# Kernel tuning notes

Measured on AMD Instinct MI355X. Metric: run time of the kernel, lower is better.

Reference implementation:

```python
import jax, jax.numpy as jnp
import numpy as np

N = 131072
H = 64
CMB_RADIUS_KM = 3485.0


def setup_inputs() -> dict:
    key = jax.random.key(0)
    ks = jax.random.split(key, 8)
    phi = jax.random.uniform(ks[0], (N, 1), jnp.float32, 0.0, 2.0 * np.pi)
    # keep theta away from the poles so sin(theta) != 0
    theta = jax.random.uniform(ks[1], (N, 1), jnp.float32, 0.1, np.pi - 0.1)
    radius = jnp.full((N, 1), CMB_RADIUS_KM, dtype=jnp.float32)
    horiz_theta = jax.random.normal(ks[2], (N, 1), jnp.float32) * 0.01
    horiz_phi = jax.random.normal(ks[3], (N, 1), jnp.float32) * 0.01
    br = jax.random.normal(ks[4], (N, 1), jnp.float32) * 100.0
    W1 = jax.random.normal(ks[5], (2, H), jnp.float32) / np.sqrt(2.0)
    b1 = jnp.zeros((H,), jnp.float32)
    W2 = jax.random.normal(ks[6], (H, H), jnp.float32) / np.sqrt(H)
    b2 = jnp.zeros((H,), jnp.float32)
    W3 = jax.random.normal(ks[7], (H, 1), jnp.float32) / np.sqrt(H)
    b3 = jnp.zeros((1,), jnp.float32)
    return dict(phi=phi, theta=theta, radius=radius, horiz_theta=horiz_theta,
                horiz_phi=horiz_phi, br=br, W1=W1, b1=b1, W2=W2, b2=b2, W3=W3, b3=b3)


def reference(phi, theta, radius, horiz_theta, horiz_phi, br, W1, b1, W2, b2, W3, b3):
    sin = jnp.sin

    # per-point scalar network; input order matches torch.cat([phi, theta], dim=1)
    def T(p, t):
        x = jnp.stack([p, t])
        h = jnp.tanh(x @ W1 + b1)
        h = jnp.tanh(h @ W2 + b2)
        return (h @ W3 + b3)[0]

    dTp = jax.grad(T, 0)
    dTt = jax.grad(T, 1)

    # In the torch code T = model(X) and P = model(X) are the same function,
    # so T_x == P_x and the flows simplify to:
    def u_th(p, t):
        return dTp(p, t) / sin(t) + dTt(p, t)

    def u_ph(p, t):
        return dTp(p, t) / sin(t) - dTt(p, t)

    # nested derivatives exactly as the chained autograd.grad calls
    u_th_t = jax.grad(lambda p, t: -u_th(p, t) * sin(t), 1)            # u_theta_theta
    u_th_tt = jax.grad(lambda p, t: u_th_t(p, t) * sin(t), 1)          # u_theta_theta_theta
    u_th_p = jax.grad(lambda p, t: -u_th(p, t), 0)                     # u_theta_phi
    u_th_pp = jax.grad(u_th_p, 0)                                      # u_theta_phi_phi
    u_ph_t = jax.grad(lambda p, t: u_ph(p, t) * sin(t), 1)             # u_phi_theta
    u_ph_tt = jax.grad(lambda p, t: u_ph_t(p, t) * sin(t), 1)          # u_phi_theta_theta
    u_ph_p = jax.grad(u_ph, 0)                                         # u_phi_phi
    u_ph_pp = jax.grad(u_ph_p, 0)                                      # u_phi_phi_phi

    def per_point(p, t):
        return (u_th(p, t), u_ph(p, t), u_th_t(p, t), u_th_tt(p, t),
                u_th_pp(p, t), u_ph_tt(p, t), u_ph_p(p, t), u_ph_pp(p, t))

    vals = jax.vmap(per_point)(phi.ravel(), theta.ravel())
    ut, up, utt, uttt, utpp, uphtt, upp, uppp = [v.reshape(-1, 1) for v in vals]

    s = sin(theta)
    div_uh = (utt + upp) / (radius * s)
    u_theta_lap = s / radius ** 2 * uttt + utpp / (radius * s) ** 2
    u_phi_lap = s / radius ** 2 * uphtt + uppp / (radius * s) ** 2
    comp = s * (u_theta_lap ** 2 + u_phi_lap ** 2)
    sv_out = -(ut * horiz_theta + up * horiz_phi) - br * div_uh
    tg_con = div_uh - ut * jnp.tan(theta) / radius
    return (ut, up, div_uh, sv_out, tg_con, comp)
```

## Files before the change

kernel.cpp:

```cpp
#include <hip/hip_runtime.h>

#define NH 64

typedef _Float16 half8 __attribute__((ext_vector_type(8)));
typedef float float4v __attribute__((ext_vector_type(4)));

__device__ __forceinline__ float fast_tanh(float x) {
  float ax = fabsf(x);
  float e  = __expf(-2.0f * ax);
  float y  = (1.0f - e) * __builtin_amdgcn_rcpf(1.0f + e);
  return copysignf(y, x);
}

__global__ void prep_B(const float* __restrict__ W2, _Float16* __restrict__ ws) {
  int i = blockIdx.x * 256 + threadIdx.x;
  if (i >= 2 * 4096) return;
  int s = i >> 12;
  int off = i & 4095;
  int nt = off >> 10;
  int ks = (off >> 9) & 1;
  int ln = (off >> 3) & 63;
  int jj = off & 7;
  int h = ks * 32 + (ln >> 4) * 8 + jj;
  int j = nt * 16 + (ln & 15);
  float w2 = W2[h * NH + j];
  _Float16 hi = (_Float16)w2;
  ws[(s * 8 + nt * 2 + ks) * 512 + ln * 8 + jj] =
      (s == 0) ? hi : (_Float16)(w2 - (float)hi);
}

__device__ __forceinline__ half8 ldB(const _Float16* ws, int s, int nt, int ks, int lane) {
  return *(const half8*)(ws + (s * 8 + nt * 2 + ks) * 512 + lane * 8);
}

__global__ __launch_bounds__(256) __attribute__((amdgpu_waves_per_eu(2, 2)))
void pinn_mfma(
    const float* __restrict__ phi, const float* __restrict__ theta,
    const float* __restrict__ radius, const float* __restrict__ hth,
    const float* __restrict__ hph, const float* __restrict__ br,
    const float* __restrict__ W1, const float* __restrict__ b1,
    const float* __restrict__ b2, const float* __restrict__ W3,
    const _Float16* __restrict__ Bws, float* __restrict__ out, int n) {
  const int lane = threadIdx.x & 63;
  const int wave = threadIdx.x >> 6;
  const int tile = blockIdx.x * 4 + wave;
  const int quad = lane >> 4, col = lane & 15;
  const int pbase = tile * 16;
  if (pbase >= n) return;

  float p = phi[pbase + col], t = theta[pbase + col];
  half8 A0h[2], A0l[2], A1h[2], A1l[2], A2h[2], A2l[2];
  half8 A3[2], A4[2], A5[2], A6[2], A7[2], A8[2], A9[2];
#pragma unroll
  for (int ks = 0; ks < 2; ++ks) {
#pragma unroll
    for (int jj = 0; jj < 8; ++jj) {
      int h = ks * 32 + quad * 8 + jj;
      float a = W1[h], b = W1[NH + h];
      float z = fmaf(p, a, fmaf(t, b, b1[h]));
      float y = fast_tanh(z);
      float f1 = fmaf(-y, y, 1.0f);
      float f2a = y * f1;
      float f3 = f1 * fmaf(-6.0f, f1, 4.0f);
      float a2 = a * a, ab = a * b, b2v_ = b * b;
      float v1 = f1 * a, v2 = f1 * b;
      _Float16 yh = (_Float16)y;
      _Float16 v1h = (_Float16)v1;
      _Float16 v2h = (_Float16)v2;
      A0h[ks][jj] = yh;   A0l[ks][jj] = (_Float16)(y - (float)yh);
      A1h[ks][jj] = v1h;  A1l[ks][jj] = (_Float16)(v1 - (float)v1h);
      A2h[ks][jj] = v2h;  A2l[ks][jj] = (_Float16)(v2 - (float)v2h);
      A3[ks][jj] = (_Float16)(f2a * (-2.0f * a2));
      A4[ks][jj] = (_Float16)(f2a * (-2.0f * ab));
      A5[ks][jj] = (_Float16)(f2a * (-2.0f * b2v_));
      A6[ks][jj] = (_Float16)(f3 * (a2 * a));
      A7[ks][jj] = (_Float16)(f3 * (a2 * b));
      A8[ks][jj] = (_Float16)(f3 * (a * b2v_));
      A9[ks][jj] = (_Float16)(f3 * (b2v_ * b));
    }
  }

  float4v Tacc[9];
#pragma unroll
  for (int x = 0; x < 9; ++x) Tacc[x] = (float4v){0.f, 0.f, 0.f, 0.f};

#pragma unroll
  for (int nt = 0; nt < 4; ++nt) {
    float4v acc[10];
#pragma unroll
    for (int k = 0; k < 10; ++k) acc[k] = (float4v){0.f, 0.f, 0.f, 0.f};
#pragma unroll
    for (int ks = 0; ks < 2; ++ks) {
      half8 bh = ldB(Bws, 0, nt, ks, lane);
      half8 bl = ldB(Bws, 1, nt, ks, lane);
      acc[0] = __builtin_amdgcn_mfma_f32_16x16x32_f16(A0h[ks], bh, acc[0], 0, 0, 0);
      acc[0] = __builtin_amdgcn_mfma_f32_16x16x32_f16(A0l[ks], bh, acc[0], 0, 0, 0);
      acc[0] = __builtin_amdgcn_mfma_f32_16x16x32_f16(A0h[ks], bl, acc[0], 0, 0, 0);
      acc[1] = __builtin_amdgcn_mfma_f32_16x16x32_f16(A1h[ks], bh, acc[1], 0, 0, 0);
      acc[1] = __builtin_amdgcn_mfma_f32_16x16x32_f16(A1l[ks], bh, acc[1], 0, 0, 0);
      acc[1] = __builtin_amdgcn_mfma_f32_16x16x32_f16(A1h[ks], bl, acc[1], 0, 0, 0);
      acc[2] = __builtin_amdgcn_mfma_f32_16x16x32_f16(A2h[ks], bh, acc[2], 0, 0, 0);
      acc[2] = __builtin_amdgcn_mfma_f32_16x16x32_f16(A2l[ks], bh, acc[2], 0, 0, 0);
      acc[2] = __builtin_amdgcn_mfma_f32_16x16x32_f16(A2h[ks], bl, acc[2], 0, 0, 0);
      acc[3] = __builtin_amdgcn_mfma_f32_16x16x32_f16(A3[ks], bh, acc[3], 0, 0, 0);
      acc[4] = __builtin_amdgcn_mfma_f32_16x16x32_f16(A4[ks], bh, acc[4], 0, 0, 0);
      acc[5] = __builtin_amdgcn_mfma_f32_16x16x32_f16(A5[ks], bh, acc[5], 0, 0, 0);
      acc[6] = __builtin_amdgcn_mfma_f32_16x16x32_f16(A6[ks], bh, acc[6], 0, 0, 0);
      acc[7] = __builtin_amdgcn_mfma_f32_16x16x32_f16(A7[ks], bh, acc[7], 0, 0, 0);
      acc[8] = __builtin_amdgcn_mfma_f32_16x16x32_f16(A8[ks], bh, acc[8], 0, 0, 0);
      acc[9] = __builtin_amdgcn_mfma_f32_16x16x32_f16(A9[ks], bh, acc[9], 0, 0, 0);
    }
    float b2v = b2[nt * 16 + col];
    float w3v = W3[nt * 16 + col];
#pragma unroll
    for (int r = 0; r < 4; ++r) {
      float z0 = acc[0][r] + b2v;
      float y2 = fast_tanh(z0);
      float g1 = fmaf(-y2, y2, 1.0f);
      float g2 = -2.0f * (y2 * g1);
      float g3 = g1 * fmaf(-6.0f, g1, 4.0f);
      float gp = acc[1][r], gt = acc[2][r];
      float gpp = acc[3][r], gpt = acc[4][r], gtt = acc[5][r];
      float zppp = acc[6][r], zppt = acc[7][r], zptt = acc[8][r], zttt = acc[9][r];
      float gp2 = gp * gp, gt2 = gt * gt;
      Tacc[0][r] = fmaf(w3v, g1 * gp, Tacc[0][r]);
      Tacc[1][r] = fmaf(w3v, g1 * gt, Tacc[1][r]);
      Tacc[2][r] = fmaf(w3v, fmaf(g2, gp2, g1 * gpp), Tacc[2][r]);
      Tacc[3][r] = fmaf(w3v, fmaf(g2, gp * gt, g1 * gpt), Tacc[3][r]);
      Tacc[4][r] = fmaf(w3v, fmaf(g2, gt2, g1 * gtt), Tacc[4][r]);
      Tacc[5][r] = fmaf(w3v, fmaf(g3, gp2 * gp, fmaf(3.0f * g2, gp * gpp, g1 * zppp)), Tacc[5][r]);
      Tacc[6][r] = fmaf(w3v, fmaf(g3, gp2 * gt, fmaf(g2, fmaf(2.0f, gp * gpt, gt * gpp), g1 * zppt)), Tacc[6][r]);
      Tacc[7][r] = fmaf(w3v, fmaf(g3, gp * gt2, fmaf(g2, fmaf(2.0f, gt * gpt, gp * gtt), g1 * zptt)), Tacc[7][r]);
      Tacc[8][r] = fmaf(w3v, fmaf(g3, gt2 * gt, fmaf(3.0f * g2, gt * gtt, g1 * zttt)), Tacc[8][r]);
    }
  }

#pragma unroll
  for (int x = 0; x < 9; ++x) {
#pragma unroll
    for (int r = 0; r < 4; ++r) {
      float v = Tacc[x][r];
      v += __shfl_xor(v, 1, 16);
      v += __shfl_xor(v, 2, 16);
      v += __shfl_xor(v, 4, 16);
      v += __shfl_xor(v, 8, 16);
      Tacc[x][r] = v;
    }
  }

  int rsel = col & 3;
  float T[9];
#pragma unroll
  for (int x = 0; x < 9; ++x) {
    float4v v = Tacc[x];
    T[x] = (rsel == 0) ? v[0] : (rsel == 1) ? v[1] : (rsel == 2) ? v[2] : v[3];
  }
  float Tp = T[0], Tt = T[1], Tpp = T[2], Tpt = T[3], Ttt = T[4];
  float Tppp = T[5], Tppt = T[6], Tptt = T[7], Tttt = T[8];

  int pi = pbase + quad * 4 + rsel;
  float t2 = theta[pi];
  float s = sinf(t2), c = cosf(t2);
  float inv_s = 1.0f / s;
  float inv_s2 = inv_s * inv_s;

  float A = Tp * inv_s + Tt;
  float D = Tp * inv_s - Tt;
  float q1 = Tpt * inv_s - Tp * c * inv_s2;
  float A_t = q1 + Ttt;
  float D_t = q1 - Ttt;
  float q2 = Tptt * inv_s - 2.0f * Tpt * c * inv_s2
           + Tp * (s * s + 2.0f * c * c) * inv_s2 * inv_s;
  float A_tt = q2 + Tttt;
  float D_tt = q2 - Tttt;
  float A_pp = Tppp * inv_s + Tppt;
  float D_p  = Tpp * inv_s - Tpt;
  float D_pp = Tppp * inv_s - Tppt;

  float utt   = -(A_t * s + A * c);
  float uttt  = -(A_tt * s + 2.0f * A_t * c - A * s) * s + utt * c;
  float utpp  = -A_pp;
  float upht  = D_t * s + D * c;
  float uphtt = (D_tt * s + 2.0f * D_t * c - D * s) * s + upht * c;
  float upp   = D_p;
  float uppp  = D_pp;

  float r = radius[pi];
  float inv_r = 1.0f / r;
  float inv_r2 = inv_r * inv_r;
  float div_uh = (utt + upp) * inv_r * inv_s;
  float lap_t = s * inv_r2 * uttt + utpp * inv_s2 * inv_r2;
  float lap_p = s * inv_r2 * uphtt + uppp * inv_s2 * inv_r2;
  float comp = s * (lap_t * lap_t + lap_p * lap_p);
  float sv = -(A * hth[pi] + D * hph[pi]) - br[pi] * div_uh;
  float tg = div_uh - A * (s / c) * inv_r;

  if (col < 4) {
    out[pi]         = A;
    out[n + pi]     = D;
    out[2 * n + pi] = div_uh;
    out[3 * n + pi] = sv;
    out[4 * n + pi] = tg;
    out[5 * n + pi] = comp;
  }
}

extern "C" void kernel_launch(void* const* d_in, const int* in_sizes, int n_in,
                              void* d_out, int out_size, void* d_ws, size_t ws_size,
                              hipStream_t stream) {
  const float* phi    = (const float*)d_in[0];
  const float* theta  = (const float*)d_in[1];
  const float* radius = (const float*)d_in[2];
  const float* hth    = (const float*)d_in[3];
  const float* hph    = (const float*)d_in[4];
  const float* br     = (const float*)d_in[5];
  const float* W1     = (const float*)d_in[6];
  const float* b1     = (const float*)d_in[7];
  const float* W2     = (const float*)d_in[8];
  const float* b2     = (const float*)d_in[9];
  const float* W3     = (const float*)d_in[10];
  (void)ws_size; (void)n_in; (void)out_size;

  _Float16* Bws = (_Float16*)d_ws;
  float* out = (float*)d_out;
  int n = in_sizes[0];

  prep_B<<<(2 * 4096 + 255) / 256, 256, 0, stream>>>(W2, Bws);
  int ntiles = (n + 15) / 16;
  int nblocks = (ntiles + 3) / 4;
  pinn_mfma<<<nblocks, 256, 0, stream>>>(
      phi, theta, radius, hth, hph, br, W1, b1, b2, W3, Bws, out, n);
}
```

Baseline: 113.2 us.

## Use transpose-reduce across lanes and fast sincos/rcp in epilogue

```diff
diff --git a/kernel.cpp b/kernel.cpp
--- a/kernel.cpp
+++ b/kernel.cpp
@@ -60,9 +60,10 @@
       float z = fmaf(p, a, fmaf(t, b, b1[h]));
       float y = fast_tanh(z);
       float f1 = fmaf(-y, y, 1.0f);
-      float f2a = y * f1;
       float f3 = f1 * fmaf(-6.0f, f1, 4.0f);
-      float a2 = a * a, ab = a * b, b2v_ = b * b;
+      float na = -2.0f * (y * f1);
+      float a2 = a * a, ab = a * b, bb = b * b;
+      float f3a2 = f3 * a2, f3bb = f3 * bb;
       float v1 = f1 * a, v2 = f1 * b;
       _Float16 yh = (_Float16)y;
       _Float16 v1h = (_Float16)v1;
@@ -70,13 +71,13 @@
       A0h[ks][jj] = yh;   A0l[ks][jj] = (_Float16)(y - (float)yh);
       A1h[ks][jj] = v1h;  A1l[ks][jj] = (_Float16)(v1 - (float)v1h);
       A2h[ks][jj] = v2h;  A2l[ks][jj] = (_Float16)(v2 - (float)v2h);
-      A3[ks][jj] = (_Float16)(f2a * (-2.0f * a2));
-      A4[ks][jj] = (_Float16)(f2a * (-2.0f * ab));
-      A5[ks][jj] = (_Float16)(f2a * (-2.0f * b2v_));
-      A6[ks][jj] = (_Float16)(f3 * (a2 * a));
-      A7[ks][jj] = (_Float16)(f3 * (a2 * b));
-      A8[ks][jj] = (_Float16)(f3 * (a * b2v_));
-      A9[ks][jj] = (_Float16)(f3 * (b2v_ * b));
+      A3[ks][jj] = (_Float16)(na * a2);
+      A4[ks][jj] = (_Float16)(na * ab);
+      A5[ks][jj] = (_Float16)(na * bb);
+      A6[ks][jj] = (_Float16)(f3a2 * a);
+      A7[ks][jj] = (_Float16)(f3a2 * b);
+      A8[ks][jj] = (_Float16)(f3bb * a);
+      A9[ks][jj] = (_Float16)(f3bb * b);
     }
   }
 
@@ -135,33 +136,34 @@
     }
   }
 
-#pragma unroll
-  for (int x = 0; x < 9; ++x) {
-#pragma unroll
-    for (int r = 0; r < 4; ++r) {
-      float v = Tacc[x][r];
-      v += __shfl_xor(v, 1, 16);
-      v += __shfl_xor(v, 2, 16);
-      v += __shfl_xor(v, 4, 16);
-      v += __shfl_xor(v, 8, 16);
-      Tacc[x][r] = v;
-    }
-  }
-
-  int rsel = col & 3;
   float T[9];
 #pragma unroll
   for (int x = 0; x < 9; ++x) {
     float4v v = Tacc[x];
-    T[x] = (rsel == 0) ? v[0] : (rsel == 1) ? v[1] : (rsel == 2) ? v[2] : v[3];
+    bool hi8 = (col & 8) != 0;
+    float k0 = hi8 ? v[2] : v[0];
+    float k1 = hi8 ? v[3] : v[1];
+    float s0 = hi8 ? v[0] : v[2];
+    float s1 = hi8 ? v[1] : v[3];
+    float p0 = k0 + __shfl_xor(s0, 8, 16);
+    float p1 = k1 + __shfl_xor(s1, 8, 16);
+    bool hi4 = (col & 4) != 0;
+    float kk = hi4 ? p1 : p0;
+    float ss = hi4 ? p0 : p1;
+    float q = kk + __shfl_xor(ss, 4, 16);
+    q += __shfl_xor(q, 2, 16);
+    q += __shfl_xor(q, 1, 16);
+    T[x] = q;
   }
   float Tp = T[0], Tt = T[1], Tpp = T[2], Tpt = T[3], Ttt = T[4];
   float Tppp = T[5], Tppt = T[6], Tptt = T[7], Tttt = T[8];
 
+  int rsel = col >> 2;
   int pi = pbase + quad * 4 + rsel;
   float t2 = theta[pi];
-  float s = sinf(t2), c = cosf(t2);
-  float inv_s = 1.0f / s;
+  float s, c;
+  __sincosf(t2, &s, &c);
+  float inv_s = __builtin_amdgcn_rcpf(s);
   float inv_s2 = inv_s * inv_s;
 
   float A = Tp * inv_s + Tt;
@@ -186,16 +188,16 @@
   float uppp  = D_pp;
 
   float r = radius[pi];
-  float inv_r = 1.0f / r;
+  float inv_r = __builtin_amdgcn_rcpf(r);
   float inv_r2 = inv_r * inv_r;
   float div_uh = (utt + upp) * inv_r * inv_s;
   float lap_t = s * inv_r2 * uttt + utpp * inv_s2 * inv_r2;
   float lap_p = s * inv_r2 * uphtt + uppp * inv_s2 * inv_r2;
   float comp = s * (lap_t * lap_t + lap_p * lap_p);
   float sv = -(A * hth[pi] + D * hph[pi]) - br[pi] * div_uh;
-  float tg = div_uh - A * (s / c) * inv_r;
-
-  if (col < 4) {
+  float tg = div_uh - A * s * __builtin_amdgcn_rcpf(c) * inv_r;
+
+  if ((col & 3) == 0) {
     out[pi]         = A;
     out[n + pi]     = D;
     out[2 * n + pi] = div_uh;
```

Result: faster. 110.3 us (-2.6%).
